# Optimization experiments

Measured on AMD Instinct MI355X. Metric: run time of the kernel, lower is better.

Reference implementation:

```python
import jax, jax.numpy as jnp
import numpy as np

B, T, N, E, H, MAXD = 32, 128, 42, 256, 8, 7
DH = E // H


def _hand_edges():
    left = [(0, 1), (1, 2), (2, 3), (3, 4), (0, 5), (5, 6), (6, 7), (7, 8), (0, 9), (9, 10), (10, 11), (11, 12), (0, 13), (13, 14), (14, 15), (15, 16), (0, 17), (17, 18), (18, 19), (19, 20)]
    right = [(21, 22), (22, 23), (23, 24), (24, 25), (21, 26), (26, 27), (27, 28), (28, 29), (21, 30), (30, 31), (31, 32), (32, 33), (21, 34), (34, 35), (35, 36), (36, 37), (21, 38), (38, 39), (39, 40), (40, 41)]
    tips = [(4, 8), (8, 12), (12, 16), (16, 20), (25, 29), (29, 33), (33, 37), (37, 41)]
    cross = [(0, 21)]
    return left + right + cross + tips


def _graph_constants():
    adj = np.zeros((N, N), dtype=np.float32)
    dist = np.zeros((N, N), dtype=np.float64)
    for a, b in _hand_edges():
        adj[a, b] = 1.0
        adj[b, a] = 1.0
        dist[a, b] = 1.0
        dist[b, a] = 1.0
    # exact replica of the module's single-pass Floyd-Warshall-style loop
    for k in range(N):
        for i in range(N):
            for j in range(N):
                if i != j and dist[i, k] > 0 and dist[k, j] > 0:
                    nd = dist[i, k] + dist[k, j]
                    if dist[i, j] == 0 or nd < dist[i, j]:
                        dist[i, j] = nd
    dist = np.clip(dist, 0, MAXD).astype(np.int32)
    return adj, dist


def setup_inputs() -> dict:
    key = jax.random.key(0)
    ks = jax.random.split(key, 12)
    adj_np, dist_np = _graph_constants()
    s_in = 1.0 / np.sqrt(E)
    return {
        'node_features': jax.random.normal(ks[0], (B, T, N, E), dtype=jnp.float32),
        'adjacency_matrix': jnp.asarray(adj_np),
        'distances': jnp.asarray(dist_np),
        'Wq': jax.random.normal(ks[1], (E, E), dtype=jnp.float32) * s_in,
        'bq': jnp.zeros((E,), dtype=jnp.float32),
        'Wk': jax.random.normal(ks[2], (E, E), dtype=jnp.float32) * s_in,
        'bk': jnp.zeros((E,), dtype=jnp.float32),
        'Wv': jax.random.normal(ks[3], (E, E), dtype=jnp.float32) * s_in,
        'bv': jnp.zeros((E,), dtype=jnp.float32),
        'Wo': jax.random.normal(ks[4], (E, E), dtype=jnp.float32) * s_in,
        'bo': jnp.zeros((E,), dtype=jnp.float32),
        'rel_emb': jax.random.normal(ks[5], (2 * MAXD + 1, H), dtype=jnp.float32) * 0.05,
    }


def reference(node_features, adjacency_matrix, distances, Wq, bq, Wk, bk, Wv, bv, Wo, bo, rel_emb):
    b, t, n, e = node_features.shape
    q = (node_features @ Wq + bq).reshape(b, t, n, H, DH)
    k = (node_features @ Wk + bk).reshape(b, t, n, H, DH)
    v = (node_features @ Wv + bv).reshape(b, t, n, H, DH)
    # scores: [b, t, h, i, j]
    scores = jnp.einsum('btihd,btjhd->bthij', q, k) / jnp.sqrt(jnp.float32(DH))
    # relative position bias: [n, n, h] -> [h, n, n]
    bias = rel_emb[distances]  # (N, N, H)
    scores = scores + jnp.transpose(bias, (2, 0, 1))[None, None]
    mask = (adjacency_matrix > 0).astype(jnp.float32)[None, None, None]
    scores = scores * mask + (1.0 - mask) * (-1e9)
    attn = jax.nn.softmax(scores, axis=-1)
    out = jnp.einsum('bthij,btjhd->btihd', attn, v).reshape(b, t, n, e)
    out = out @ Wo + bo
    return out, attn
```

## Files before the change

kernel.cpp:

```cpp
#include <hip/hip_runtime.h>
#include <stdint.h>


#define TPB 512
constexpr int BT = 4096;
constexpr int N = 42, NP = 48, E = 256, H = 8;
constexpr int NE = N * E;
constexpr int NN = N * N;
constexpr float SCALE = 0.17677669529663687f;

constexpr size_t WT_OFF = 0;
constexpr size_t DM_OFF = 524288;
constexpr size_t Q_OFF  = 528384;
constexpr size_t K_OFF  = Q_OFF + (size_t)BT * 48 * 256 * 2;
constexpr size_t VT_OFF = K_OFF + (size_t)BT * 48 * 256 * 2;

typedef short sh8 __attribute__((ext_vector_type(8)));
typedef float f4 __attribute__((ext_vector_type(4)));

__device__ __forceinline__ uint32_t cvtpk(float lo, float hi) {
  uint32_t d;
  asm("v_cvt_pk_bf16_f32 %0, %1, %2" : "=v"(d) : "v"(lo), "v"(hi));
  return d;
}
__device__ __forceinline__ uint16_t f2b1(float f) { return (uint16_t)cvtpk(f, f); }
__device__ __forceinline__ float b2f(uint16_t u) {
  union { uint32_t i; float f; } v; v.i = ((uint32_t)u) << 16; return v.f;
}

#define SWZ(base, row, cb) \
  ((char*)(base) + ((((row) << 9) + (cb)) ^ (((row) & 7) << 4)))

__global__ __launch_bounds__(256) void wt_kernel(
    const float* __restrict__ Wq, const float* __restrict__ Wk,
    const float* __restrict__ Wv, const float* __restrict__ Wo,
    const float* __restrict__ adj, const int* __restrict__ dist,
    uint16_t* __restrict__ WT, uint8_t* __restrict__ dm8g) {
  const int z = blockIdx.z;
  if (z == 4) {
    if (blockIdx.x == 0 && blockIdx.y == 0) {
      for (int t = threadIdx.x; t < NP * NP; t += 256) {
        const int i = t / NP, j = t - i * NP;
        uint8_t v = 0;
        if (i < N && j < N)
          v = (uint8_t)dist[i * N + j] | (adj[i * N + j] > 0.f ? 0x80 : 0);
        dm8g[t] = v;
      }
    }
    return;
  }
  __shared__ float tl[32][33];
  const float* W = (z == 0) ? Wq : (z == 1) ? Wk : (z == 2) ? Wv : Wo;
  uint16_t* dst = WT + z * 65536;
  const int k0 = blockIdx.y * 32, n0 = blockIdx.x * 32;
  const int r = threadIdx.x >> 5, cc = threadIdx.x & 31;
#pragma unroll
  for (int p = 0; p < 4; ++p)
    tl[r + 8 * p][cc] = W[(k0 + r + 8 * p) * E + n0 + cc];
  __syncthreads();
#pragma unroll
  for (int p = 0; p < 4; ++p)
    dst[(n0 + r + 8 * p) * E + k0 + cc] = f2b1(tl[cc][r + 8 * p]);
}

__device__ __forceinline__ void gemm_pass(const uint16_t* __restrict__ Wt,
                                          const char* Xb, int c, int lg, int nt0,
                                          f4 acc[3][2]) {
#pragma unroll
  for (int mt = 0; mt < 3; ++mt)
#pragma unroll
    for (int nt = 0; nt < 2; ++nt) acc[mt][nt] = (f4){0.f, 0.f, 0.f, 0.f};
  for (int kc = 0; kc < E; kc += 32) {
    sh8 xa[3];
#pragma unroll
    for (int mt = 0; mt < 3; ++mt)
      xa[mt] = *(const sh8*)SWZ(Xb, 16 * mt + c, (kc + 8 * lg) * 2);
#pragma unroll
    for (int nt = 0; nt < 2; ++nt) {
      const sh8 b8 = *(const sh8*)(Wt + ((nt0 + nt) * 16 + c) * E + kc + 8 * lg);
#pragma unroll
      for (int mt = 0; mt < 3; ++mt)
        acc[mt][nt] = __builtin_amdgcn_mfma_f32_16x16x32_bf16(xa[mt], b8, acc[mt][nt], 0, 0, 0);
    }
  }
}

__device__ __forceinline__ void frag_to_stage(const f4 acc[3][2],
                                              const float* __restrict__ bias,
                                              int n0, int c, int lg,
                                              uint16_t* __restrict__ stage) {
#pragma unroll
  for (int nt = 0; nt < 2; ++nt) {
    const int n = n0 + 16 * nt + c;
    const float bv_ = bias[n];
#pragma unroll
    for (int mt = 0; mt < 3; ++mt)
#pragma unroll
      for (int r = 0; r < 4; ++r)
        stage[(16 * mt + 4 * lg + r) * 256 + n] = f2b1(acc[mt][nt][r] + bv_);
  }
}

__global__ __launch_bounds__(TPB, 4) void qkv_kernel(
    const float* __restrict__ X,
    const float* __restrict__ bq, const float* __restrict__ bk,
    const float* __restrict__ bv, const uint16_t* __restrict__ WT,
    uint16_t* __restrict__ Qg, uint16_t* __restrict__ Kg,
    char* __restrict__ VTg) {
  alignas(16) __shared__ char Xb[NP * 512];
  alignas(16) __shared__ char stage[NP * 512];
  const int gid = blockIdx.x;
  const int tid = threadIdx.x;
  const int w = tid >> 6, lane = tid & 63, c = lane & 15, lg = lane >> 4;
  const int nt0 = 2 * w, n0 = 32 * w;

  {
    const float4* Xs = (const float4*)(X + (size_t)gid * NE);
    for (int i = tid; i < NE / 4; i += TPB) {
      const float4 v = Xs[i];
      uint2 pk; pk.x = cvtpk(v.x, v.y); pk.y = cvtpk(v.z, v.w);
      *(uint2*)SWZ(Xb, i >> 6, (i & 63) << 3) = pk;
    }
    for (int i = tid; i < (NP - N) * 64; i += TPB) {
      uint2 z; z.x = 0u; z.y = 0u;
      *(uint2*)SWZ(Xb, N + (i >> 6), (i & 63) << 3) = z;
    }
  }
  __syncthreads();

  f4 acc[3][2];
  gemm_pass(WT, Xb, c, lg, nt0, acc);
  frag_to_stage(acc, bq, n0, c, lg, (uint16_t*)stage);
  __syncthreads();
  {
    uint4* dst = (uint4*)(Qg + (size_t)gid * 12288);
    const uint4* src = (const uint4*)stage;
    for (int i = tid; i < 1536; i += TPB) dst[i] = src[i];
  }
  gemm_pass(WT + 65536, Xb, c, lg, nt0, acc);
  __syncthreads();
  frag_to_stage(acc, bk, n0, c, lg, (uint16_t*)stage);
  __syncthreads();
  {
    uint4* dst = (uint4*)(Kg + (size_t)gid * 12288);
    const uint4* src = (const uint4*)stage;
    for (int i = tid; i < 1536; i += TPB) dst[i] = src[i];
  }
  gemm_pass(WT + 131072, Xb, c, lg, nt0, acc);
  __syncthreads();
#pragma unroll
  for (int nt = 0; nt < 2; ++nt) {
    const int n = n0 + 16 * nt + c;
    const float bv_ = bv[n];
#pragma unroll
    for (int mt = 0; mt < 3; ++mt) {
      uint2 pk;
      pk.x = cvtpk(acc[mt][nt][0] + bv_, acc[mt][nt][1] + bv_);
      pk.y = cvtpk(acc[mt][nt][2] + bv_, acc[mt][nt][3] + bv_);
      *(uint2*)(stage + n * 96 + 32 * mt + 8 * lg) = pk;
    }
  }
  __syncthreads();
  {
    uint4* dst = (uint4*)(VTg + (size_t)gid * 24576);
    const uint4* src = (const uint4*)stage;
    for (int i = tid; i < 1536; i += TPB) dst[i] = src[i];
  }
}

__global__ __launch_bounds__(TPB, 4) void attn_wo_kernel(
    const float* __restrict__ bo, const float* __restrict__ rel,
    const uint16_t* __restrict__ WT, const uint16_t* __restrict__ Qg,
    const uint16_t* __restrict__ Kg, const char* __restrict__ VTg,
    const uint8_t* __restrict__ dm8g,
    float* __restrict__ out, float* __restrict__ attn) {
  alignas(16) __shared__ char smem[70368];
  char* const Ob = smem;
  uint8_t* const dm8 = (uint8_t*)(smem + 67584);
  float*   const relL = (float*)(smem + 69888);

  const int gid = blockIdx.x;
  const int tid = threadIdx.x;
  const int w = tid >> 6, lane = tid & 63, c = lane & 15, lg = lane >> 4;
  const int nt0 = 2 * w, n0 = 32 * w, h = w;
  uint16_t* const scr = (uint16_t*)(smem + 24576 + w * 5376);

  for (int t = tid; t < NP * NP; t += TPB) dm8[t] = dm8g[t];
  for (int t = tid; t < 120; t += TPB) relL[t] = rel[t];
  __syncthreads();

  sh8 qa[3], kb[3];
#pragma unroll
  for (int mt = 0; mt < 3; ++mt) {
    const size_t ro = ((size_t)gid * 48 + 16 * mt + c) * 256 + 32 * h + 8 * lg;
    qa[mt] = *(const sh8*)(Qg + ro);
    kb[mt] = *(const sh8*)(Kg + ro);
  }

  f4 st[3][3];
#pragma unroll
  for (int mt = 0; mt < 3; ++mt)
#pragma unroll
    for (int nt = 0; nt < 3; ++nt) {
      st[mt][nt] = (f4){0.f, 0.f, 0.f, 0.f};
      st[mt][nt] = __builtin_amdgcn_mfma_f32_16x16x32_bf16(kb[mt], qa[nt], st[mt][nt], 0, 0, 0);
    }

  uint16_t* const Psw = scr;
#pragma unroll
  for (int nt = 0; nt < 3; ++nt) {
    const int i = 16 * nt + c;
    float sv[12];
#pragma unroll
    for (int mt = 0; mt < 3; ++mt)
#pragma unroll
      for (int r = 0; r < 4; ++r) {
        const int j = 16 * mt + 4 * lg + r;
        const uint8_t dm = dm8[i * NP + j];
        const float s = st[mt][nt][r] * SCALE + relL[(dm & 0x7f) * 8 + h];
        sv[mt * 4 + r] = (dm & 0x80) ? s : -1e9f;
      }
    float m = sv[0];
#pragma unroll
    for (int k = 1; k < 12; ++k) m = fmaxf(m, sv[k]);
    m = fmaxf(m, __shfl_xor(m, 16));
    m = fmaxf(m, __shfl_xor(m, 32));
    float p[12], sum = 0.f;
#pragma unroll
    for (int k = 0; k < 12; ++k) { p[k] = __expf(sv[k] - m); sum += p[k]; }
    sum += __shfl_xor(sum, 16);
    sum += __shfl_xor(sum, 32);
    const float inv = __builtin_amdgcn_rcpf(sum);
#pragma unroll
    for (int mt = 0; mt < 3; ++mt) {
      const uint32_t d0 = cvtpk(p[mt * 4 + 0] * inv, p[mt * 4 + 1] * inv);
      const uint32_t d1 = cvtpk(p[mt * 4 + 2] * inv, p[mt * 4 + 3] * inv);
      char* base = (char*)Psw + i * 112 + 32 * mt + 8 * lg;
      *(uint32_t*)base = d0;
      *(uint32_t*)(base + 4) = d1;
    }
  }

  {
    const size_t abase = ((size_t)gid * H + h) * (size_t)NN;
    for (int p = lane; p < NN; p += 64) {
      const int i = p / N, j = p - i * N;
      attn[abase + p] = b2f(Psw[i * 56 + j]);
    }
  }

  const sh8 z8 = {0, 0, 0, 0, 0, 0, 0, 0};
  sh8 pa0[3], pa1[3], vb0[2], vb1[2];
#pragma unroll
  for (int mt = 0; mt < 3; ++mt) {
    char* base = (char*)Psw + (16 * mt + c) * 112;
    pa0[mt] = *(const sh8*)(base + 16 * lg);
    pa1[mt] = (lg < 2) ? *(const sh8*)(base + 64 + 16 * lg) : z8;
  }
#pragma unroll
  for (int nt = 0; nt < 2; ++nt) {
    const char* base = VTg + (size_t)gid * 24576 + (h * 32 + 16 * nt + c) * 96;
    vb0[nt] = *(const sh8*)(base + 16 * lg);
    vb1[nt] = (lg < 2) ? *(const sh8*)(base + 64 + 16 * lg) : z8;
  }
  f4 ov[3][2];
#pragma unroll
  for (int mt = 0; mt < 3; ++mt)
#pragma unroll
    for (int nt = 0; nt < 2; ++nt) {
      ov[mt][nt] = (f4){0.f, 0.f, 0.f, 0.f};
      ov[mt][nt] = __builtin_amdgcn_mfma_f32_16x16x32_bf16(pa0[mt], vb0[nt], ov[mt][nt], 0, 0, 0);
      ov[mt][nt] = __builtin_amdgcn_mfma_f32_16x16x32_bf16(pa1[mt], vb1[nt], ov[mt][nt], 0, 0, 0);
    }

#pragma unroll
  for (int mt = 0; mt < 3; ++mt)
#pragma unroll
    for (int nt = 0; nt < 2; ++nt)
#pragma unroll
      for (int r = 0; r < 4; ++r)
        *(uint16_t*)SWZ(Ob, 16 * mt + 4 * lg + r, (n0 + 16 * nt + c) * 2) =
            f2b1(ov[mt][nt][r]);
  __syncthreads();

  {
    f4 ao[3][2];
    gemm_pass(WT + 196608, Ob, c, lg, nt0, ao);
#pragma unroll
    for (int nt = 0; nt < 2; ++nt) {
      const int n = n0 + 16 * nt + c;
      const float bov = bo[n];
#pragma unroll
      for (int mt = 0; mt < 3; ++mt)
#pragma unroll
        for (int r = 0; r < 4; ++r) {
          const int i = 16 * mt + 4 * lg + r;
          if (i < N) out[(size_t)gid * NE + i * E + n] = ao[mt][nt][r] + bov;
        }
    }
  }
}

extern "C" void kernel_launch(void* const* d_in, const int* in_sizes, int n_in,
                              void* d_out, int out_size, void* d_ws, size_t ws_size,
                              hipStream_t stream) {
  const float* X    = (const float*)d_in[0];
  const float* adj  = (const float*)d_in[1];
  const int*   dist = (const int*)d_in[2];
  const float* Wq   = (const float*)d_in[3];
  const float* bq   = (const float*)d_in[4];
  const float* Wk   = (const float*)d_in[5];
  const float* bk   = (const float*)d_in[6];
  const float* Wv   = (const float*)d_in[7];
  const float* bv   = (const float*)d_in[8];
  const float* Wo   = (const float*)d_in[9];
  const float* bo   = (const float*)d_in[10];
  const float* rel  = (const float*)d_in[11];
  float* out  = (float*)d_out;
  float* attn = out + (size_t)BT * NE;

  char* ws = (char*)d_ws;
  uint16_t* WT   = (uint16_t*)(ws + WT_OFF);
  uint8_t*  dm8g = (uint8_t*)(ws + DM_OFF);
  uint16_t* Qg   = (uint16_t*)(ws + Q_OFF);
  uint16_t* Kg   = (uint16_t*)(ws + K_OFF);
  char*     VTg  = ws + VT_OFF;

  wt_kernel<<<dim3(8, 8, 5), dim3(256), 0, stream>>>(Wq, Wk, Wv, Wo, adj, dist, WT, dm8g);
  qkv_kernel<<<dim3(BT), dim3(TPB), 0, stream>>>(X, bq, bk, bv, WT, Qg, Kg, VTg);
  attn_wo_kernel<<<dim3(BT), dim3(TPB), 0, stream>>>(bo, rel, WT, Qg, Kg, VTg, dm8g, out, attn);
}
```

Measured before the change: 441.3 us.

## Fuse Q/K/V projection GEMMs into one K-loop with double-buffered staging

The QKV kernel now computes the Q, K and V projections in a single pass over the K dimension. Each LDS read of the X fragment feeds three MFMA chains, where before there were three separate gemm_pass calls. A second LDS staging buffer lets the copy-out of one projection overlap with staging the next, which removes some barriers. In exchange it holds three accumulator sets in registers, so launch bounds drop to 2 blocks per CU and LDS use rises, which lowers occupancy.

```diff
diff --git a/kernel.cpp b/kernel.cpp
--- a/kernel.cpp
+++ b/kernel.cpp
@@ -101,18 +101,27 @@
   }
 }
 
-__global__ __launch_bounds__(TPB, 4) void qkv_kernel(
+__device__ __forceinline__ void copy_out(const char* __restrict__ stage,
+                                         char* __restrict__ dst, int tid) {
+  const uint4* src = (const uint4*)stage;
+  uint4* d = (uint4*)dst;
+  for (int i = tid; i < 1536; i += TPB) d[i] = src[i];
+}
+
+__global__ __launch_bounds__(TPB, 2) void qkv_kernel(
     const float* __restrict__ X,
     const float* __restrict__ bq, const float* __restrict__ bk,
     const float* __restrict__ bv, const uint16_t* __restrict__ WT,
     uint16_t* __restrict__ Qg, uint16_t* __restrict__ Kg,
     char* __restrict__ VTg) {
   alignas(16) __shared__ char Xb[NP * 512];
-  alignas(16) __shared__ char stage[NP * 512];
+  alignas(16) __shared__ char stageA[NP * 512];
+  alignas(16) __shared__ char stageB[NP * 512];
   const int gid = blockIdx.x;
   const int tid = threadIdx.x;
   const int w = tid >> 6, lane = tid & 63, c = lane & 15, lg = lane >> 4;
   const int nt0 = 2 * w, n0 = 32 * w;
+  (void)lane;
 
   {
     const float4* Xs = (const float4*)(X + (size_t)gid * NE);
@@ -128,25 +137,39 @@
   }
   __syncthreads();
 
-  f4 acc[3][2];
-  gemm_pass(WT, Xb, c, lg, nt0, acc);
-  frag_to_stage(acc, bq, n0, c, lg, (uint16_t*)stage);
-  __syncthreads();
-  {
-    uint4* dst = (uint4*)(Qg + (size_t)gid * 12288);
-    const uint4* src = (const uint4*)stage;
-    for (int i = tid; i < 1536; i += TPB) dst[i] = src[i];
-  }
-  gemm_pass(WT + 65536, Xb, c, lg, nt0, acc);
-  __syncthreads();
-  frag_to_stage(acc, bk, n0, c, lg, (uint16_t*)stage);
-  __syncthreads();
-  {
-    uint4* dst = (uint4*)(Kg + (size_t)gid * 12288);
-    const uint4* src = (const uint4*)stage;
-    for (int i = tid; i < 1536; i += TPB) dst[i] = src[i];
-  }
-  gemm_pass(WT + 131072, Xb, c, lg, nt0, acc);
+  f4 aQ[3][2], aK[3][2], aV[3][2];
+#pragma unroll
+  for (int mt = 0; mt < 3; ++mt)
+#pragma unroll
+    for (int nt = 0; nt < 2; ++nt) {
+      aQ[mt][nt] = (f4){0.f, 0.f, 0.f, 0.f};
+      aK[mt][nt] = (f4){0.f, 0.f, 0.f, 0.f};
+      aV[mt][nt] = (f4){0.f, 0.f, 0.f, 0.f};
+    }
+  for (int kc = 0; kc < E; kc += 32) {
+    sh8 xa[3];
+#pragma unroll
+    for (int mt = 0; mt < 3; ++mt)
+      xa[mt] = *(const sh8*)SWZ(Xb, 16 * mt + c, (kc + 8 * lg) * 2);
+#pragma unroll
+    for (int nt = 0; nt < 2; ++nt) {
+      const int ko = ((nt0 + nt) * 16 + c) * E + kc + 8 * lg;
+      const sh8 bq8 = *(const sh8*)(WT + ko);
+      const sh8 bk8 = *(const sh8*)(WT + 65536 + ko);
+      const sh8 bv8 = *(const sh8*)(WT + 131072 + ko);
+#pragma unroll
+      for (int mt = 0; mt < 3; ++mt) {
+        aQ[mt][nt] = __builtin_amdgcn_mfma_f32_16x16x32_bf16(xa[mt], bq8, aQ[mt][nt], 0, 0, 0);
+        aK[mt][nt] = __builtin_amdgcn_mfma_f32_16x16x32_bf16(xa[mt], bk8, aK[mt][nt], 0, 0, 0);
+        aV[mt][nt] = __builtin_amdgcn_mfma_f32_16x16x32_bf16(xa[mt], bv8, aV[mt][nt], 0, 0, 0);
+      }
+    }
+  }
+
+  frag_to_stage(aQ, bq, n0, c, lg, (uint16_t*)stageA);
+  __syncthreads();
+  frag_to_stage(aK, bk, n0, c, lg, (uint16_t*)stageB);
+  copy_out(stageA, (char*)(Qg + (size_t)gid * 12288), tid);
   __syncthreads();
 #pragma unroll
   for (int nt = 0; nt < 2; ++nt) {
@@ -155,17 +178,14 @@
 #pragma unroll
     for (int mt = 0; mt < 3; ++mt) {
       uint2 pk;
-      pk.x = cvtpk(acc[mt][nt][0] + bv_, acc[mt][nt][1] + bv_);
-      pk.y = cvtpk(acc[mt][nt][2] + bv_, acc[mt][nt][3] + bv_);
-      *(uint2*)(stage + n * 96 + 32 * mt + 8 * lg) = pk;
-    }
-  }
-  __syncthreads();
-  {
-    uint4* dst = (uint4*)(VTg + (size_t)gid * 24576);
-    const uint4* src = (const uint4*)stage;
-    for (int i = tid; i < 1536; i += TPB) dst[i] = src[i];
-  }
+      pk.x = cvtpk(aV[mt][nt][0] + bv_, aV[mt][nt][1] + bv_);
+      pk.y = cvtpk(aV[mt][nt][2] + bv_, aV[mt][nt][3] + bv_);
+      *(uint2*)(stageA + n * 96 + 32 * mt + 8 * lg) = pk;
+    }
+  }
+  copy_out(stageB, (char*)(Kg + (size_t)gid * 12288), tid);
+  __syncthreads();
+  copy_out(stageA, VTg + (size_t)gid * 24576, tid);
 }
 
 __global__ __launch_bounds__(TPB, 4) void attn_wo_kernel(
```

Result: slower. 477.4 us (+8.2%).

## Make QKV kernel persistent with register-prefetched, double-buffered input tiles

Applied to the files above, without the earlier changes.

The QKV projection kernel now launches a fixed grid of 512 blocks that loop over the 4096 (b,t) tiles. While the three projection GEMMs run on the current tile, the next tile's fp32 inputs are prefetched into registers, then converted to bf16 into a second LDS buffer. This aims to hide global load latency behind compute. The cost is 24 extra registers for the prefetch and a larger LDS footprint, which may lower occupancy, and the smaller grid may underfill the 256 CUs.

```diff
diff --git a/kernel.cpp b/kernel.cpp
--- a/kernel.cpp
+++ b/kernel.cpp
@@ -7,6 +7,7 @@
 constexpr int N = 42, NP = 48, E = 256, H = 8;
 constexpr int NE = N * E;
 constexpr int NN = N * N;
+constexpr int QGRID = 512;
 constexpr float SCALE = 0.17677669529663687f;
 
 constexpr size_t WT_OFF = 0;
@@ -101,70 +102,96 @@
   }
 }
 
+__device__ __forceinline__ void copy_out(const char* __restrict__ stage,
+                                         char* __restrict__ dst, int tid) {
+  const uint4* src = (const uint4*)stage;
+  uint4* d = (uint4*)dst;
+  for (int i = tid; i < 1536; i += TPB) d[i] = src[i];
+}
+
 __global__ __launch_bounds__(TPB, 4) void qkv_kernel(
     const float* __restrict__ X,
     const float* __restrict__ bq, const float* __restrict__ bk,
     const float* __restrict__ bv, const uint16_t* __restrict__ WT,
     uint16_t* __restrict__ Qg, uint16_t* __restrict__ Kg,
     char* __restrict__ VTg) {
-  alignas(16) __shared__ char Xb[NP * 512];
+  alignas(16) __shared__ char XbBuf[2][NP * 512];
   alignas(16) __shared__ char stage[NP * 512];
-  const int gid = blockIdx.x;
   const int tid = threadIdx.x;
-  const int w = tid >> 6, lane = tid & 63, c = lane & 15, lg = lane >> 4;
+  const int w = tid >> 6, c = (tid & 63) & 15, lg = (tid & 63) >> 4;
   const int nt0 = 2 * w, n0 = 32 * w;
 
+#pragma unroll
+  for (int b = 0; b < 2; ++b)
+    for (int i = tid; i < (NP - N) * 64; i += TPB) {
+      uint2 z; z.x = 0u; z.y = 0u;
+      *(uint2*)SWZ(XbBuf[b], N + (i >> 6), (i & 63) << 3) = z;
+    }
   {
-    const float4* Xs = (const float4*)(X + (size_t)gid * NE);
+    const float4* Xs = (const float4*)(X + (size_t)blockIdx.x * NE);
     for (int i = tid; i < NE / 4; i += TPB) {
       const float4 v = Xs[i];
       uint2 pk; pk.x = cvtpk(v.x, v.y); pk.y = cvtpk(v.z, v.w);
-      *(uint2*)SWZ(Xb, i >> 6, (i & 63) << 3) = pk;
-    }
-    for (int i = tid; i < (NP - N) * 64; i += TPB) {
-      uint2 z; z.x = 0u; z.y = 0u;
-      *(uint2*)SWZ(Xb, N + (i >> 6), (i & 63) << 3) = z;
+      *(uint2*)SWZ(XbBuf[0], i >> 6, (i & 63) << 3) = pk;
     }
   }
   __syncthreads();
 
-  f4 acc[3][2];
-  gemm_pass(WT, Xb, c, lg, nt0, acc);
-  frag_to_stage(acc, bq, n0, c, lg, (uint16_t*)stage);
-  __syncthreads();
-  {
-    uint4* dst = (uint4*)(Qg + (size_t)gid * 12288);
-    const uint4* src = (const uint4*)stage;
-    for (int i = tid; i < 1536; i += TPB) dst[i] = src[i];
-  }
-  gemm_pass(WT + 65536, Xb, c, lg, nt0, acc);
-  __syncthreads();
-  frag_to_stage(acc, bk, n0, c, lg, (uint16_t*)stage);
-  __syncthreads();
-  {
-    uint4* dst = (uint4*)(Kg + (size_t)gid * 12288);
-    const uint4* src = (const uint4*)stage;
-    for (int i = tid; i < 1536; i += TPB) dst[i] = src[i];
-  }
-  gemm_pass(WT + 131072, Xb, c, lg, nt0, acc);
-  __syncthreads();
-#pragma unroll
-  for (int nt = 0; nt < 2; ++nt) {
-    const int n = n0 + 16 * nt + c;
-    const float bv_ = bv[n];
-#pragma unroll
-    for (int mt = 0; mt < 3; ++mt) {
-      uint2 pk;
-      pk.x = cvtpk(acc[mt][nt][0] + bv_, acc[mt][nt][1] + bv_);
-      pk.y = cvtpk(acc[mt][nt][2] + bv_, acc[mt][nt][3] + bv_);
-      *(uint2*)(stage + n * 96 + 32 * mt + 8 * lg) = pk;
-    }
-  }
-  __syncthreads();
-  {
-    uint4* dst = (uint4*)(VTg + (size_t)gid * 24576);
-    const uint4* src = (const uint4*)stage;
-    for (int i = tid; i < 1536; i += TPB) dst[i] = src[i];
+  int cur = 0;
+  for (int g = blockIdx.x; g < BT; g += QGRID) {
+    const int gn = g + QGRID;
+    const bool pv = gn < BT;
+    float4 xpre[6];
+    if (pv) {
+      const float4* Xs = (const float4*)(X + (size_t)gn * NE);
+#pragma unroll
+      for (int t = 0; t < 6; ++t) {
+        const int i = tid + TPB * t;
+        if (i < NE / 4) xpre[t] = Xs[i];
+      }
+    }
+
+    const char* const Xb = XbBuf[cur];
+    f4 acc[3][2];
+    gemm_pass(WT, Xb, c, lg, nt0, acc);
+    frag_to_stage(acc, bq, n0, c, lg, (uint16_t*)stage);
+    __syncthreads();
+    copy_out(stage, (char*)(Qg + (size_t)g * 12288), tid);
+    gemm_pass(WT + 65536, Xb, c, lg, nt0, acc);
+    __syncthreads();
+    frag_to_stage(acc, bk, n0, c, lg, (uint16_t*)stage);
+    __syncthreads();
+    copy_out(stage, (char*)(Kg + (size_t)g * 12288), tid);
+    gemm_pass(WT + 131072, Xb, c, lg, nt0, acc);
+    __syncthreads();
+#pragma unroll
+    for (int nt = 0; nt < 2; ++nt) {
+      const int n = n0 + 16 * nt + c;
+      const float bv_ = bv[n];
+#pragma unroll
+      for (int mt = 0; mt < 3; ++mt) {
+        uint2 pk;
+        pk.x = cvtpk(acc[mt][nt][0] + bv_, acc[mt][nt][1] + bv_);
+        pk.y = cvtpk(acc[mt][nt][2] + bv_, acc[mt][nt][3] + bv_);
+        *(uint2*)(stage + n * 96 + 32 * mt + 8 * lg) = pk;
+      }
+    }
+    __syncthreads();
+    copy_out(stage, VTg + (size_t)g * 24576, tid);
+
+    if (pv) {
+#pragma unroll
+      for (int t = 0; t < 6; ++t) {
+        const int i = tid + TPB * t;
+        if (i < NE / 4) {
+          uint2 pk; pk.x = cvtpk(xpre[t].x, xpre[t].y);
+          pk.y = cvtpk(xpre[t].z, xpre[t].w);
+          *(uint2*)SWZ(XbBuf[cur ^ 1], i >> 6, (i & 63) << 3) = pk;
+        }
+      }
+    }
+    __syncthreads();
+    cur ^= 1;
   }
 }
 
@@ -327,6 +354,6 @@
   char*     VTg  = ws + VT_OFF;
 
   wt_kernel<<<dim3(8, 8, 5), dim3(256), 0, stream>>>(Wq, Wk, Wv, Wo, adj, dist, WT, dm8g);
-  qkv_kernel<<<dim3(BT), dim3(TPB), 0, stream>>>(X, bq, bk, bv, WT, Qg, Kg, VTg);
+  qkv_kernel<<<dim3(QGRID), dim3(TPB), 0, stream>>>(X, bq, bk, bv, WT, Qg, Kg, VTg);
   attn_wo_kernel<<<dim3(BT), dim3(TPB), 0, stream>>>(bo, rel, WT, Qg, Kg, VTg, dm8g, out, attn);
 }
```

Result: slower. 618.6 us (+40.2%).
